# Optimization experiments

Hardware: AMD Instinct MI355X
Metric: run time of the kernel (lower is better)

The kernel has to match this reference:

```python
import jax, jax.numpy as jnp
import numpy as np

L = 4            # n_layers
D_MODEL = 768
D_STATE = 16
D_CONV = 4
EXPAND = 2
D_INNER = EXPAND * D_MODEL      # 1536
DT_RANK = (D_MODEL + 15) // 16  # 48
B = 2
T = 2048
LN_EPS = 1e-5


def setup_inputs() -> dict:
    key = jax.random.key(0)
    ks = jax.random.split(key, 12)
    s = 0.02
    x = jax.random.normal(ks[0], (B, T, D_MODEL), dtype=jnp.float32)
    in_proj_w = jax.random.normal(ks[1], (L, 2 * D_INNER, D_MODEL), dtype=jnp.float32) * s
    conv_w = jax.random.normal(ks[2], (L, D_INNER, D_CONV), dtype=jnp.float32) * s
    conv_b = jnp.zeros((L, D_INNER), dtype=jnp.float32)
    x_proj_w = jax.random.normal(ks[3], (L, DT_RANK + 2 * D_STATE, D_INNER), dtype=jnp.float32) * s
    dt_proj_w = jax.random.normal(ks[4], (L, D_INNER, DT_RANK), dtype=jnp.float32) * s
    dt_proj_b = jax.random.normal(ks[5], (L, D_INNER), dtype=jnp.float32) * 0.1
    # Standard S4D-real init: A = -[1..d_state], stored as log
    A_log = jnp.log(jnp.broadcast_to(
        jnp.arange(1, D_STATE + 1, dtype=jnp.float32), (L, D_INNER, D_STATE)))
    D_param = jnp.ones((L, D_INNER), dtype=jnp.float32)
    out_proj_w = jax.random.normal(ks[6], (L, D_MODEL, D_INNER), dtype=jnp.float32) * s
    ln_g = jnp.ones((L, D_MODEL), dtype=jnp.float32)
    ln_b = jnp.zeros((L, D_MODEL), dtype=jnp.float32)
    return {"x": x, "in_proj_w": in_proj_w, "conv_w": conv_w, "conv_b": conv_b,
            "x_proj_w": x_proj_w, "dt_proj_w": dt_proj_w, "dt_proj_b": dt_proj_b,
            "A_log": A_log, "D_param": D_param, "out_proj_w": out_proj_w,
            "ln_g": ln_g, "ln_b": ln_b}


def _layernorm(x, g, b):
    mu = jnp.mean(x, axis=-1, keepdims=True)
    var = jnp.mean(jnp.square(x - mu), axis=-1, keepdims=True)
    return (x - mu) * jax.lax.rsqrt(var + LN_EPS) * g + b


def _mamba_layer(x, inw, convw, convb, xpw, dtw, dtb, A_log, Dp, outw):
    # x: [B,T,d_model]
    Tn = x.shape[1]
    xz = jnp.einsum('btd,ed->bte', x, inw)          # [B,T,2*d_inner]
    xin, z = jnp.split(xz, 2, axis=-1)              # each [B,T,d_inner]
    # causal depthwise conv1d over time (kernel d_conv)
    xp = jnp.pad(xin, ((0, 0), (D_CONV - 1, 0), (0, 0)))
    xc = convb
    for k in range(D_CONV):
        xc = xc + xp[:, k:k + Tn, :] * convw[:, k]
    xc = jax.nn.silu(xc)                            # [B,T,d_inner]
    dbl = jnp.einsum('bti,ei->bte', xc, xpw)        # [B,T,dt_rank+2*d_state]
    dt, Bs, Cs = jnp.split(dbl, [DT_RANK, DT_RANK + D_STATE], axis=-1)
    dt = jax.nn.softplus(jnp.einsum('btr,dr->btd', dt, dtw) + dtb)  # [B,T,d_inner]
    A = -jnp.exp(A_log)                             # [d_inner,d_state]
    dA = jnp.exp(jnp.einsum('btd,dn->btdn', dt, A))  # discretized A
    dBu = (dt * xc)[..., None] * Bs[:, :, None, :]   # [B,T,d_inner,d_state]

    def step(h, inp):
        dA_t, dBu_t, C_t = inp                      # [B,d,n],[B,d,n],[B,n]
        h = dA_t * h + dBu_t
        y = jnp.einsum('bdn,bn->bd', h, C_t)
        return h, y

    h0 = jnp.zeros((x.shape[0], D_INNER, D_STATE), x.dtype)
    _, ys = jax.lax.scan(step, h0,
                         (jnp.swapaxes(dA, 0, 1), jnp.swapaxes(dBu, 0, 1),
                          jnp.swapaxes(Cs, 0, 1)))
    y = jnp.swapaxes(ys, 0, 1) + xc * Dp            # skip connection D*u
    y = y * jax.nn.silu(z)                          # gate
    return jnp.einsum('bti,ei->bte', y, outw)       # [B,T,d_model]


def reference(x, in_proj_w, conv_w, conv_b, x_proj_w, dt_proj_w, dt_proj_b,
              A_log, D_param, out_proj_w, ln_g, ln_b):
    for l in range(L):
        residual = x
        h = _mamba_layer(x, in_proj_w[l], conv_w[l], conv_b[l], x_proj_w[l],
                         dt_proj_w[l], dt_proj_b[l], A_log[l], D_param[l],
                         out_proj_w[l])
        h = _layernorm(h, ln_g[l], ln_b[l])
        x = h + residual                            # dropout=0 -> identity
    return x
```

## Files before the change

kernel.cpp:

```cpp
#include <hip/hip_runtime.h>

#define T_LEN 2048
#define DM    768
#define DI    1536
#define DS    16
#define BB    2
#define NROWS (BB * T_LEN)
#define NCH   128
#define CLEN  16

#define OFF_DTB 0
#define OFF_A   6144
#define OFF_DP  104448
#define OFF_CW  110592
#define OFF_CB  135168
#define OFF_LG  141312
#define OFF_LB  144384
#define PRM_TOT 147456

typedef __attribute__((ext_vector_type(8))) short bh8;
typedef __attribute__((ext_vector_type(4))) float f32x4;

typedef const __attribute__((address_space(1))) void as1_void;
typedef __attribute__((address_space(3))) void as3_void;

__device__ __forceinline__ void glds16(const void* g, void* l) {
    __builtin_amdgcn_global_load_lds((as1_void*)g, (as3_void*)l, 16, 0, 0);
}

__device__ __forceinline__ float bf2f(unsigned short u) {
    return __uint_as_float(((unsigned)u) << 16);
}
__device__ __forceinline__ unsigned short f2bf(float f) {
    unsigned u = __float_as_uint(f);
    u += 0x7FFFu + ((u >> 16) & 1u);
    return (unsigned short)(u >> 16);
}
__device__ __forceinline__ float ldin(const void* p, long i, int bf) {
    return bf ? bf2f(((const unsigned short*)p)[i]) : ((const float*)p)[i];
}

__global__ void k_sniff(const unsigned short* __restrict__ x, int* __restrict__ flag) {
    __shared__ int cnt[4];
    int tid = threadIdx.x;
    int local = 0;
#pragma unroll
    for (int j = 0; j < 4; ++j) {
        unsigned short u = x[tid * 4 + j];
        int e = (u >> 7) & 0xFF;
        if (e >= 100 && e <= 140) local++;
    }
    for (int off = 32; off; off >>= 1) local += __shfl_down(local, off, 64);
    if ((tid & 63) == 0) cnt[tid >> 6] = local;
    __syncthreads();
    if (tid == 0) {
        int tot = cnt[0] + cnt[1] + cnt[2] + cnt[3];
        *flag = (tot >= 900) ? 1 : 0;
    }
}

__global__ void k_conv_bf16(unsigned short* __restrict__ dst, const void* __restrict__ src,
                            long n, const int* __restrict__ flag) {
    int bf = *flag;
    long i = (long)blockIdx.x * 256 + threadIdx.x;
    if (i < n) dst[i] = bf ? ((const unsigned short*)src)[i] : f2bf(((const float*)src)[i]);
}

__global__ void k_convx(unsigned short* __restrict__ xbf, float* __restrict__ xf,
                        const void* __restrict__ src, const int* __restrict__ flag) {
    int bf = *flag;
    long i = (long)blockIdx.x * 256 + threadIdx.x;
    if (i < (long)NROWS * DM) {
        float v = ldin(src, i, bf);
        xbf[i] = f2bf(v);
        xf[i]  = v;
    }
}

__global__ void k_conv_xpw(unsigned short* __restrict__ dst, const void* __restrict__ src,
                           const int* __restrict__ flag) {
    int bf = *flag;
    long i = (long)blockIdx.x * 256 + threadIdx.x;
    const long total = 4L * 128 * 1536;
    if (i < total) {
        int c = (int)(i % 1536);
        long rl = i / 1536;
        int r = (int)(rl % 128);
        int l = (int)(rl / 128);
        unsigned short v = 0;
        if (r < 80) {
            long si = ((long)l * 80 + r) * 1536 + c;
            v = bf ? ((const unsigned short*)src)[si] : f2bf(((const float*)src)[si]);
        }
        dst[i] = v;
    }
}

__global__ void k_conv_dtw(unsigned short* __restrict__ dst, const void* __restrict__ src,
                           const int* __restrict__ flag) {
    int bf = *flag;
    long i = (long)blockIdx.x * 256 + threadIdx.x;
    const long total = 4L * 1536 * 64;
    if (i < total) {
        int c = (int)(i % 64);
        long rl = i / 64;
        int d = (int)(rl % 1536);
        int l = (int)(rl / 1536);
        unsigned short v = 0;
        if (c < 48) {
            long si = ((long)l * 1536 + d) * 48 + c;
            v = bf ? ((const unsigned short*)src)[si] : f2bf(((const float*)src)[si]);
        }
        dst[i] = v;
    }
}

__global__ void k_params(float* __restrict__ prm, const void* dtb, const void* alog,
                         const void* dpar, const void* cw, const void* cb,
                         const void* lg, const void* lb, const int* __restrict__ flag) {
    int bf = *flag;
    int i = blockIdx.x * 256 + threadIdx.x;
    if (i >= PRM_TOT) return;
    float v;
    if (i < OFF_A)        v = ldin(dtb, i - OFF_DTB, bf);
    else if (i < OFF_DP)  v = -__expf(ldin(alog, i - OFF_A, bf));
    else if (i < OFF_CW)  v = ldin(dpar, i - OFF_DP, bf);
    else if (i < OFF_CB)  v = ldin(cw, i - OFF_CW, bf);
    else if (i < OFF_LG)  v = ldin(cb, i - OFF_CB, bf);
    else if (i < OFF_LB)  v = ldin(lg, i - OFF_LG, bf);
    else                  v = ldin(lb, i - OFF_LB, bf);
    prm[i] = v;
}

__global__ __launch_bounds__(256) void k_gemm128(const unsigned short* __restrict__ A,
                                                 const unsigned short* __restrict__ B,
                                                 float* __restrict__ C,
                                                 int M, int N, int K) {
    __shared__ __align__(16) unsigned short As[128 * 32];
    __shared__ __align__(16) unsigned short Bs[128 * 32];
    const int tid = threadIdx.x;
    const int lane = tid & 63, wid = tid >> 6;
    const int wm = wid >> 1, wn = wid & 1;
    const long arow0 = (long)blockIdx.y * 128;
    const long bcol0 = (long)blockIdx.x * 128;
    const int r16 = lane >> 2;
    const int c8  = (lane & 3) * 8;
    f32x4 acc[4][4] = {};

    for (int k0 = 0; k0 < K; k0 += 32) {
#pragma unroll
        for (int j = 0; j < 2; ++j) {
            int chunk = wid + j * 4;
            int row = chunk * 16 + r16;
            glds16(&A[(arow0 + row) * K + k0 + c8], &As[chunk * 512]);
            glds16(&B[(bcol0 + row) * K + k0 + c8], &Bs[chunk * 512]);
        }
        __syncthreads();
        const int row = lane & 15, q8 = (lane >> 4) * 8;
        bh8 af[4], bfr[4];
#pragma unroll
        for (int i = 0; i < 4; ++i) af[i] = *(const bh8*)&As[(wm * 64 + i * 16 + row) * 32 + q8];
#pragma unroll
        for (int i = 0; i < 4; ++i) bfr[i] = *(const bh8*)&Bs[(wn * 64 + i * 16 + row) * 32 + q8];
#pragma unroll
        for (int i = 0; i < 4; ++i)
#pragma unroll
            for (int j = 0; j < 4; ++j)
                acc[i][j] = __builtin_amdgcn_mfma_f32_16x16x32_bf16(af[i], bfr[j], acc[i][j], 0, 0, 0);
        __syncthreads();
    }
    const int crow = (lane >> 4) * 4, ccol = lane & 15;
#pragma unroll
    for (int i = 0; i < 4; ++i)
#pragma unroll
        for (int j = 0; j < 4; ++j)
#pragma unroll
            for (int r = 0; r < 4; ++r) {
                long gr = arow0 + wm * 64 + i * 16 + crow + r;
                long gc = bcol0 + wn * 64 + j * 16 + ccol;
                C[gr * N + gc] = acc[i][j][r];
            }
}

template <int EPI>
__global__ __launch_bounds__(256) void k_gemm64(const unsigned short* __restrict__ A,
                                                const unsigned short* __restrict__ B,
                                                float* __restrict__ C,
                                                int M, int N, int K,
                                                const float* __restrict__ bias,
                                                unsigned short* __restrict__ dtlr) {
    __shared__ __align__(16) unsigned short As[64 * 32];
    __shared__ __align__(16) unsigned short Bs[64 * 32];
    const int tid = threadIdx.x;
    const int lane = tid & 63, wid = tid >> 6;
    const int wm = wid >> 1, wn = wid & 1;
    const long arow0 = (long)blockIdx.y * 64;
    const long bcol0 = (long)blockIdx.x * 64;
    const int r16 = lane >> 2;
    const int c8  = (lane & 3) * 8;
    f32x4 acc[2][2] = {};

    for (int k0 = 0; k0 < K; k0 += 32) {
        int row = wid * 16 + r16;
        glds16(&A[(arow0 + row) * K + k0 + c8], &As[wid * 512]);
        glds16(&B[(bcol0 + row) * K + k0 + c8], &Bs[wid * 512]);
        __syncthreads();
        const int row2 = lane & 15, q8 = (lane >> 4) * 8;
        bh8 af[2], bfr[2];
#pragma unroll
        for (int i = 0; i < 2; ++i) af[i] = *(const bh8*)&As[(wm * 32 + i * 16 + row2) * 32 + q8];
#pragma unroll
        for (int i = 0; i < 2; ++i) bfr[i] = *(const bh8*)&Bs[(wn * 32 + i * 16 + row2) * 32 + q8];
#pragma unroll
        for (int i = 0; i < 2; ++i)
#pragma unroll
            for (int j = 0; j < 2; ++j)
                acc[i][j] = __builtin_amdgcn_mfma_f32_16x16x32_bf16(af[i], bfr[j], acc[i][j], 0, 0, 0);
        __syncthreads();
    }
    const int crow = (lane >> 4) * 4, ccol = lane & 15;
#pragma unroll
    for (int i = 0; i < 2; ++i)
#pragma unroll
        for (int j = 0; j < 2; ++j)
#pragma unroll
            for (int r = 0; r < 4; ++r) {
                long gr = arow0 + wm * 32 + i * 16 + crow + r;
                long gc = bcol0 + wn * 32 + j * 16 + ccol;
                float v = acc[i][j][r];
                if (EPI == 1) {
                    v += bias[gc];
                    v = (v > 20.f) ? v : log1pf(__expf(v));
                }
                C[gr * N + gc] = v;
                if (EPI == 2) {
                    if (gc < 64) dtlr[gr * 64 + gc] = (gc < 48) ? f2bf(v) : (unsigned short)0;
                }
            }
}

__global__ __launch_bounds__(256) void k_conv(const float* __restrict__ xz,
                                              const float* __restrict__ cw,
                                              const float* __restrict__ cb,
                                              unsigned short* __restrict__ xcbf) {
    long i = (long)blockIdx.x * 256 + threadIdx.x;
    if (i >= (long)NROWS * DI) return;
    int d = (int)(i % DI);
    long bt = i / DI;
    int t = (int)(bt & (T_LEN - 1));
    float acc = cb[d];
#pragma unroll
    for (int k = 0; k < 4; ++k) {
        int ts = t + k - 3;
        if (ts >= 0) acc += xz[(bt + k - 3) * (2 * DI) + d] * cw[d * 4 + k];
    }
    float s = acc / (1.f + __expf(-acc));
    xcbf[i] = f2bf(s);
}

__global__ __launch_bounds__(256) void k_scan1(const float* __restrict__ dt,
                                               const unsigned short* __restrict__ xcbf,
                                               const float* __restrict__ dbl,
                                               const float* __restrict__ An,
                                               float* __restrict__ hch,
                                               float* __restrict__ sdtb) {
    const int tid = threadIdx.x;
    const int db = blockIdx.x % 6;
    const int c  = (blockIdx.x / 6) % NCH;
    const int b  = blockIdx.x / (6 * NCH);
    const int d  = db * 256 + tid;
    const int t0 = c * CLEN;
    float h[DS], An_r[DS];
    const f32x4* Ap = (const f32x4*)(An + (long)d * DS);
#pragma unroll
    for (int q = 0; q < 4; ++q) {
        f32x4 a4 = Ap[q];
#pragma unroll
        for (int j = 0; j < 4; ++j) { An_r[q * 4 + j] = a4[j]; h[q * 4 + j] = 0.f; }
    }
    float sdt = 0.f;
    const long rowb = (long)b * T_LEN + t0;
#pragma unroll 4
    for (int s = 0; s < CLEN; ++s) {
        long bt = rowb + s;
        float dtv = dt[bt * DI + d];
        float xcv = bf2f(xcbf[bt * DI + d]);
        int bi = __builtin_amdgcn_readfirstlane((int)(bt * 128 + 48));
        const f32x4* bp = (const f32x4*)(dbl + bi);
        float Bv[DS];
#pragma unroll
        for (int q = 0; q < 4; ++q) {
            f32x4 b4 = bp[q];
#pragma unroll
            for (int j = 0; j < 4; ++j) Bv[q * 4 + j] = b4[j];
        }
        float du = dtv * xcv;
        sdt += dtv;
#pragma unroll
        for (int n = 0; n < DS; ++n)
            h[n] = __expf(An_r[n] * dtv) * h[n] + du * Bv[n];
    }
    long o = (((long)b * NCH + c) * DI + d) * DS;
    f32x4* hp = (f32x4*)(hch + o);
#pragma unroll
    for (int q = 0; q < 4; ++q) {
        f32x4 h4;
#pragma unroll
        for (int j = 0; j < 4; ++j) h4[j] = h[q * 4 + j];
        hp[q] = h4;
    }
    sdtb[((long)b * NCH + c) * DI + d] = sdt;
}

__global__ __launch_bounds__(256) void k_scan2(float* __restrict__ hbuf,
                                               const float* __restrict__ sdtb,
                                               const float* __restrict__ An) {
    long gid = (long)blockIdx.x * 256 + threadIdx.x;
    if (gid >= (long)BB * DI * DS) return;
    int n = (int)(gid & 15);
    long r = gid >> 4;
    int d = (int)(r % DI);
    int b = (int)(r / DI);
    float an = An[(long)d * DS + n];
    float h = 0.f;
    for (int c = 0; c < NCH; ++c) {
        long idx = (((long)b * NCH + c) * DI + d) * DS + n;
        float p = __expf(an * sdtb[((long)b * NCH + c) * DI + d]);
        float g = hbuf[idx];
        hbuf[idx] = h;
        h = p * h + g;
    }
}

__global__ __launch_bounds__(256) void k_scan3(const float* __restrict__ dt,
                                               const unsigned short* __restrict__ xcbf,
                                               const float* __restrict__ dbl,
                                               const float* __restrict__ An,
                                               const float* __restrict__ Dp,
                                               const float* __restrict__ hin,
                                               const float* __restrict__ xz,
                                               unsigned short* __restrict__ ybf) {
    const int tid = threadIdx.x;
    const int db = blockIdx.x % 6;
    const int c  = (blockIdx.x / 6) % NCH;
    const int b  = blockIdx.x / (6 * NCH);
    const int d  = db * 256 + tid;
    const int t0 = c * CLEN;
    float h[DS], An_r[DS];
    long o = (((long)b * NCH + c) * DI + d) * DS;
    const f32x4* Ap = (const f32x4*)(An + (long)d * DS);
    const f32x4* Hp = (const f32x4*)(hin + o);
#pragma unroll
    for (int q = 0; q < 4; ++q) {
        f32x4 a4 = Ap[q], h4 = Hp[q];
#pragma unroll
        for (int j = 0; j < 4; ++j) { An_r[q * 4 + j] = a4[j]; h[q * 4 + j] = h4[j]; }
    }
    const float dcoef = Dp[d];
    const long rowb = (long)b * T_LEN + t0;
#pragma unroll 4
    for (int s = 0; s < CLEN; ++s) {
        long bt = rowb + s;
        float dtv = dt[bt * DI + d];
        float xcv = bf2f(xcbf[bt * DI + d]);
        int bi = __builtin_amdgcn_readfirstlane((int)(bt * 128 + 48));
        const f32x4* bp = (const f32x4*)(dbl + bi);
        float Bv[DS], Cv[DS];
#pragma unroll
        for (int q = 0; q < 4; ++q) {
            f32x4 b4 = bp[q], c4 = bp[q + 4];
#pragma unroll
            for (int j = 0; j < 4; ++j) { Bv[q * 4 + j] = b4[j]; Cv[q * 4 + j] = c4[j]; }
        }
        float du = dtv * xcv;
        float yp[4] = {xcv * dcoef, 0.f, 0.f, 0.f};
#pragma unroll
        for (int n = 0; n < DS; ++n) {
            h[n] = __expf(An_r[n] * dtv) * h[n] + du * Bv[n];
            yp[n & 3] += h[n] * Cv[n];
        }
        float y = (yp[0] + yp[1]) + (yp[2] + yp[3]);
        float zv = xz[bt * (2 * DI) + DI + d];
        y *= zv / (1.f + __expf(-zv));
        ybf[bt * DI + d] = f2bf(y);
    }
}

__global__ __launch_bounds__(256) void k_ln(const float* __restrict__ prj,
                                            float* __restrict__ x,
                                            unsigned short* __restrict__ xbf,
                                            const float* __restrict__ lg,
                                            const float* __restrict__ lb,
                                            void* __restrict__ dout,
                                            int is_last, const int* __restrict__ flag) {
    __shared__ float red[8];
    const int row = blockIdx.x;
    const int tid = threadIdx.x;
    float v[3];
    float s = 0.f, s2 = 0.f;
#pragma unroll
    for (int j = 0; j < 3; ++j) {
        v[j] = prj[(long)row * DM + tid + j * 256];
        s += v[j];
        s2 += v[j] * v[j];
    }
    for (int off = 32; off; off >>= 1) {
        s  += __shfl_down(s, off, 64);
        s2 += __shfl_down(s2, off, 64);
    }
    if ((tid & 63) == 0) { red[tid >> 6] = s; red[4 + (tid >> 6)] = s2; }
    __syncthreads();
    float S  = red[0] + red[1] + red[2] + red[3];
    float S2 = red[4] + red[5] + red[6] + red[7];
    float mu = S * (1.f / DM);
    float var = S2 * (1.f / DM) - mu * mu;
    float rs = rsqrtf(var + 1e-5f);
    int bf = *flag;
#pragma unroll
    for (int j = 0; j < 3; ++j) {
        int e = tid + j * 256;
        long idx = (long)row * DM + e;
        float out = (v[j] - mu) * rs * lg[e] + lb[e] + x[idx];
        x[idx] = out;
        xbf[idx] = f2bf(out);
        if (is_last) {
            if (bf) ((unsigned short*)dout)[idx] = f2bf(out);
            else    ((float*)dout)[idx] = out;
        }
    }
}

extern "C" void kernel_launch(void* const* d_in, const int* in_sizes, int n_in,
                              void* d_out, int out_size, void* d_ws, size_t ws_size,
                              hipStream_t stream) {
    char* ws = (char*)d_ws;
    const size_t O_FLAG = 0;
    const size_t O_WIN  = 256;
    const size_t O_WXP  = O_WIN + 18874368;
    const size_t O_WDT  = O_WXP + 1572864;
    const size_t O_WOUT = O_WDT + 786432;
    const size_t O_PRM  = O_WOUT + 9437184;
    const size_t O_XBF  = O_PRM + 589824;
    const size_t O_XF   = O_XBF + 6291456;
    const size_t O_XZ   = O_XF + 12582912;
    const size_t O_XCBF = O_XZ + 50331648;
    const size_t O_DBL  = O_XCBF + 12582912;
    const size_t O_DTLR = O_DBL + 2097152;
    const size_t O_DT   = O_DTLR + 524288;
    const size_t O_HCH  = O_DT + 25165824;
    const size_t O_SDT  = O_HCH + 25165824;
    const size_t O_YBF  = O_SDT + 1572864;

    int* flag = (int*)(ws + O_FLAG);
    unsigned short* Win  = (unsigned short*)(ws + O_WIN);
    unsigned short* Wxp  = (unsigned short*)(ws + O_WXP);
    unsigned short* Wdt  = (unsigned short*)(ws + O_WDT);
    unsigned short* Wout = (unsigned short*)(ws + O_WOUT);
    float* prm = (float*)(ws + O_PRM);
    unsigned short* Xbf = (unsigned short*)(ws + O_XBF);
    float* Xf  = (float*)(ws + O_XF);
    float* Xz  = (float*)(ws + O_XZ);
    unsigned short* Xcbf = (unsigned short*)(ws + O_XCBF);
    float* Dbl = (float*)(ws + O_DBL);
    unsigned short* Dtlr = (unsigned short*)(ws + O_DTLR);
    float* Dt  = (float*)(ws + O_DT);
    float* Hch = (float*)(ws + O_HCH);
    float* Sdt = (float*)(ws + O_SDT);
    unsigned short* Ybf = (unsigned short*)(ws + O_YBF);
    float* Prj = Xz;

    const void* in_x   = d_in[0];
    const void* in_inw = d_in[1];
    const void* in_xpw = d_in[4];
    const void* in_dtw = d_in[5];
    const void* in_ow  = d_in[9];

    k_sniff<<<1, 256, 0, stream>>>((const unsigned short*)in_x, flag);
    k_convx<<<12288, 256, 0, stream>>>(Xbf, Xf, in_x, flag);
    k_conv_bf16<<<36864, 256, 0, stream>>>(Win, in_inw, 9437184L, flag);
    k_conv_bf16<<<18432, 256, 0, stream>>>(Wout, in_ow, 4718592L, flag);
    k_conv_xpw<<<3072, 256, 0, stream>>>(Wxp, in_xpw, flag);
    k_conv_dtw<<<1536, 256, 0, stream>>>(Wdt, in_dtw, flag);
    k_params<<<576, 256, 0, stream>>>(prm, d_in[6], d_in[7], d_in[8], d_in[2], d_in[3],
                                      d_in[10], d_in[11], flag);

    for (int l = 0; l < 4; ++l) {
        const unsigned short* winL  = Win  + (size_t)l * 3072 * 768;
        const unsigned short* wxpL  = Wxp  + (size_t)l * 128 * 1536;
        const unsigned short* wdtL  = Wdt  + (size_t)l * 1536 * 64;
        const unsigned short* woutL = Wout + (size_t)l * 768 * 1536;
        const float* cwL  = prm + OFF_CW  + (size_t)l * DI * 4;
        const float* cbL  = prm + OFF_CB  + (size_t)l * DI;
        const float* dtbL = prm + OFF_DTB + (size_t)l * DI;
        const float* anL  = prm + OFF_A   + (size_t)l * DI * DS;
        const float* dpL  = prm + OFF_DP  + (size_t)l * DI;
        const float* lgL  = prm + OFF_LG  + (size_t)l * DM;
        const float* lbL  = prm + OFF_LB  + (size_t)l * DM;

        k_gemm128<<<dim3(24, 32), 256, 0, stream>>>(Xbf, winL, Xz, NROWS, 2 * DI, DM);
        k_conv<<<24576, 256, 0, stream>>>(Xz, cwL, cbL, Xcbf);
        k_gemm64<2><<<dim3(2, 64), 256, 0, stream>>>(Xcbf, wxpL, Dbl, NROWS, 128, DI, nullptr, Dtlr);
        k_gemm64<1><<<dim3(24, 64), 256, 0, stream>>>(Dtlr, wdtL, Dt, NROWS, DI, 64, dtbL, nullptr);
        k_scan1<<<BB * NCH * 6, 256, 0, stream>>>(Dt, Xcbf, Dbl, anL, Hch, Sdt);
        k_scan2<<<192, 256, 0, stream>>>(Hch, Sdt, anL);
        k_scan3<<<BB * NCH * 6, 256, 0, stream>>>(Dt, Xcbf, Dbl, anL, dpL, Hch, Xz, Ybf);
        k_gemm64<0><<<dim3(12, 64), 256, 0, stream>>>(Ybf, woutL, Prj, NROWS, DM, DI, nullptr, nullptr);
        k_ln<<<4096, 256, 0, stream>>>(Prj, Xf, Xbf, lgL, lbL, d_out, (l == 3) ? 1 : 0, flag);
    }
}
```

Baseline: 1.021 ms.

## Store intermediates in bf16, split-K x_proj, two-level chunk scan, tiled conv, fused prep

The in_proj output and dt are now stored in bf16 instead of fp32, which halves the intermediate traffic through conv and the scans. x_proj becomes a split-K GEMM that accumulates with atomicAdd into a zeroed buffer, giving more blocks for a skinny output. dt_proj now reads fp32 Dbl directly and converts it to bf16 in LDS, which removes the separate Dtlr buffer. The sequential inter-chunk scan is split into a segmented pass plus a short cross-segment pass to raise parallelism. The depthwise conv is tiled through LDS, and the six weight-prep kernels are merged into one launch. The costs are extra bf16 rounding of xz and dt, nondeterministic atomic summation, and an added memset.

```diff
diff --git a/kernel.cpp b/kernel.cpp
--- a/kernel.cpp
+++ b/kernel.cpp
@@ -8,6 +8,8 @@
 #define NROWS (BB * T_LEN)
 #define NCH   128
 #define CLEN  16
+#define NSEG  8
+#define SEGC  16
 
 #define OFF_DTB 0
 #define OFF_A   6144
@@ -59,30 +61,34 @@
     }
 }
 
-__global__ void k_conv_bf16(unsigned short* __restrict__ dst, const void* __restrict__ src,
-                            long n, const int* __restrict__ flag) {
+__global__ void k_prep(const void* in_x, const void* in_inw, const void* in_ow,
+                       const void* in_xpw, const void* in_dtw,
+                       const void* dtb, const void* alog, const void* dpar,
+                       const void* cw, const void* cb, const void* lg, const void* lb,
+                       unsigned short* __restrict__ xbf, float* __restrict__ xf,
+                       unsigned short* __restrict__ Win, unsigned short* __restrict__ Wout,
+                       unsigned short* __restrict__ Wxp, unsigned short* __restrict__ Wdt,
+                       float* __restrict__ prm, const int* __restrict__ flag) {
+    const long E0 = 3145728L;
+    const long E1 = E0 + 9437184L;
+    const long E2 = E1 + 4718592L;
+    const long E3 = E2 + 786432L;
+    const long E4 = E3 + 393216L;
+    const long E5 = E4 + 147456L;
     int bf = *flag;
-    long i = (long)blockIdx.x * 256 + threadIdx.x;
-    if (i < n) dst[i] = bf ? ((const unsigned short*)src)[i] : f2bf(((const float*)src)[i]);
-}
-
-__global__ void k_convx(unsigned short* __restrict__ xbf, float* __restrict__ xf,
-                        const void* __restrict__ src, const int* __restrict__ flag) {
-    int bf = *flag;
-    long i = (long)blockIdx.x * 256 + threadIdx.x;
-    if (i < (long)NROWS * DM) {
-        float v = ldin(src, i, bf);
-        xbf[i] = f2bf(v);
-        xf[i]  = v;
-    }
-}
-
-__global__ void k_conv_xpw(unsigned short* __restrict__ dst, const void* __restrict__ src,
-                           const int* __restrict__ flag) {
-    int bf = *flag;
-    long i = (long)blockIdx.x * 256 + threadIdx.x;
-    const long total = 4L * 128 * 1536;
-    if (i < total) {
+    long gid = (long)blockIdx.x * 256 + threadIdx.x;
+    if (gid < E0) {
+        float v = ldin(in_x, gid, bf);
+        xbf[gid] = f2bf(v);
+        xf[gid]  = v;
+    } else if (gid < E1) {
+        long i = gid - E0;
+        Win[i] = bf ? ((const unsigned short*)in_inw)[i] : f2bf(((const float*)in_inw)[i]);
+    } else if (gid < E2) {
+        long i = gid - E1;
+        Wout[i] = bf ? ((const unsigned short*)in_ow)[i] : f2bf(((const float*)in_ow)[i]);
+    } else if (gid < E3) {
+        long i = gid - E2;
         int c = (int)(i % 1536);
         long rl = i / 1536;
         int r = (int)(rl % 128);
@@ -90,18 +96,11 @@
         unsigned short v = 0;
         if (r < 80) {
             long si = ((long)l * 80 + r) * 1536 + c;
-            v = bf ? ((const unsigned short*)src)[si] : f2bf(((const float*)src)[si]);
-        }
-        dst[i] = v;
-    }
-}
-
-__global__ void k_conv_dtw(unsigned short* __restrict__ dst, const void* __restrict__ src,
-                           const int* __restrict__ flag) {
-    int bf = *flag;
-    long i = (long)blockIdx.x * 256 + threadIdx.x;
-    const long total = 4L * 1536 * 64;
-    if (i < total) {
+            v = bf ? ((const unsigned short*)in_xpw)[si] : f2bf(((const float*)in_xpw)[si]);
+        }
+        Wxp[i] = v;
+    } else if (gid < E4) {
+        long i = gid - E3;
         int c = (int)(i % 64);
         long rl = i / 64;
         int d = (int)(rl % 1536);
@@ -109,32 +108,26 @@
         unsigned short v = 0;
         if (c < 48) {
             long si = ((long)l * 1536 + d) * 48 + c;
-            v = bf ? ((const unsigned short*)src)[si] : f2bf(((const float*)src)[si]);
-        }
-        dst[i] = v;
-    }
-}
-
-__global__ void k_params(float* __restrict__ prm, const void* dtb, const void* alog,
-                         const void* dpar, const void* cw, const void* cb,
-                         const void* lg, const void* lb, const int* __restrict__ flag) {
-    int bf = *flag;
-    int i = blockIdx.x * 256 + threadIdx.x;
-    if (i >= PRM_TOT) return;
-    float v;
-    if (i < OFF_A)        v = ldin(dtb, i - OFF_DTB, bf);
-    else if (i < OFF_DP)  v = -__expf(ldin(alog, i - OFF_A, bf));
-    else if (i < OFF_CW)  v = ldin(dpar, i - OFF_DP, bf);
-    else if (i < OFF_CB)  v = ldin(cw, i - OFF_CW, bf);
-    else if (i < OFF_LG)  v = ldin(cb, i - OFF_CB, bf);
-    else if (i < OFF_LB)  v = ldin(lg, i - OFF_LG, bf);
-    else                  v = ldin(lb, i - OFF_LB, bf);
-    prm[i] = v;
+            v = bf ? ((const unsigned short*)in_dtw)[si] : f2bf(((const float*)in_dtw)[si]);
+        }
+        Wdt[i] = v;
+    } else if (gid < E5) {
+        int i = (int)(gid - E4);
+        float v;
+        if (i < OFF_A)        v = ldin(dtb, i - OFF_DTB, bf);
+        else if (i < OFF_DP)  v = -__expf(ldin(alog, i - OFF_A, bf));
+        else if (i < OFF_CW)  v = ldin(dpar, i - OFF_DP, bf);
+        else if (i < OFF_CB)  v = ldin(cw, i - OFF_CW, bf);
+        else if (i < OFF_LG)  v = ldin(cb, i - OFF_CB, bf);
+        else if (i < OFF_LB)  v = ldin(lg, i - OFF_LG, bf);
+        else                  v = ldin(lb, i - OFF_LB, bf);
+        prm[i] = v;
+    }
 }
 
 __global__ __launch_bounds__(256) void k_gemm128(const unsigned short* __restrict__ A,
                                                  const unsigned short* __restrict__ B,
-                                                 float* __restrict__ C,
+                                                 unsigned short* __restrict__ C,
                                                  int M, int N, int K) {
     __shared__ __align__(16) unsigned short As[128 * 32];
     __shared__ __align__(16) unsigned short Bs[128 * 32];
@@ -178,17 +171,134 @@
             for (int r = 0; r < 4; ++r) {
                 long gr = arow0 + wm * 64 + i * 16 + crow + r;
                 long gc = bcol0 + wn * 64 + j * 16 + ccol;
-                C[gr * N + gc] = acc[i][j][r];
+                C[gr * N + gc] = f2bf(acc[i][j][r]);
             }
 }
 
-template <int EPI>
-__global__ __launch_bounds__(256) void k_gemm64(const unsigned short* __restrict__ A,
-                                                const unsigned short* __restrict__ B,
-                                                float* __restrict__ C,
-                                                int M, int N, int K,
+__global__ __launch_bounds__(256) void k_xproj(const unsigned short* __restrict__ A,
+                                               const unsigned short* __restrict__ B,
+                                               float* __restrict__ C) {
+    __shared__ __align__(16) unsigned short As[64 * 32];
+    __shared__ __align__(16) unsigned short Bs[64 * 32];
+    const int tid = threadIdx.x;
+    const int lane = tid & 63, wid = tid >> 6;
+    const int wm = wid >> 1, wn = wid & 1;
+    const long arow0 = (long)blockIdx.y * 64;
+    const long bcol0 = (long)blockIdx.x * 64;
+    const int kbase = blockIdx.z * 384;
+    const int r16 = lane >> 2;
+    const int c8  = (lane & 3) * 8;
+    f32x4 acc[2][2] = {};
+
+    for (int kk = 0; kk < 384; kk += 32) {
+        int k0 = kbase + kk;
+        int row = wid * 16 + r16;
+        glds16(&A[(arow0 + row) * DI + k0 + c8], &As[wid * 512]);
+        glds16(&B[(bcol0 + row) * DI + k0 + c8], &Bs[wid * 512]);
+        __syncthreads();
+        const int row2 = lane & 15, q8 = (lane >> 4) * 8;
+        bh8 af[2], bfr[2];
+#pragma unroll
+        for (int i = 0; i < 2; ++i) af[i] = *(const bh8*)&As[(wm * 32 + i * 16 + row2) * 32 + q8];
+#pragma unroll
+        for (int i = 0; i < 2; ++i) bfr[i] = *(const bh8*)&Bs[(wn * 32 + i * 16 + row2) * 32 + q8];
+#pragma unroll
+        for (int i = 0; i < 2; ++i)
+#pragma unroll
+            for (int j = 0; j < 2; ++j)
+                acc[i][j] = __builtin_amdgcn_mfma_f32_16x16x32_bf16(af[i], bfr[j], acc[i][j], 0, 0, 0);
+        __syncthreads();
+    }
+    const int crow = (lane >> 4) * 4, ccol = lane & 15;
+#pragma unroll
+    for (int i = 0; i < 2; ++i)
+#pragma unroll
+        for (int j = 0; j < 2; ++j)
+#pragma unroll
+            for (int r = 0; r < 4; ++r) {
+                long gr = arow0 + wm * 32 + i * 16 + crow + r;
+                long gc = bcol0 + wn * 32 + j * 16 + ccol;
+                atomicAdd(&C[gr * 128 + gc], acc[i][j][r]);
+            }
+}
+
+__global__ __launch_bounds__(256) void k_dtproj(const float* __restrict__ Dbl,
+                                                const unsigned short* __restrict__ Wdt,
                                                 const float* __restrict__ bias,
-                                                unsigned short* __restrict__ dtlr) {
+                                                unsigned short* __restrict__ Dt) {
+    __shared__ __align__(16) unsigned short As[2 * 64 * 32];
+    __shared__ __align__(16) unsigned short Bs[2 * 64 * 32];
+    const int tid = threadIdx.x;
+    const int lane = tid & 63, wid = tid >> 6;
+    const int wm = wid >> 1, wn = wid & 1;
+    const long arow0 = (long)blockIdx.y * 64;
+    const long bcol0 = (long)blockIdx.x * 64;
+
+    {
+        int r = tid >> 2;
+        int cs = (tid & 3) * 16;
+        unsigned short tmp[16];
+#pragma unroll
+        for (int q = 0; q < 4; ++q) {
+            int col0 = cs + q * 4;
+            if (col0 < 48) {
+                f32x4 v = *(const f32x4*)&Dbl[(arow0 + r) * 128 + col0];
+#pragma unroll
+                for (int j = 0; j < 4; ++j) tmp[q * 4 + j] = f2bf(v[j]);
+            } else {
+#pragma unroll
+                for (int j = 0; j < 4; ++j) tmp[q * 4 + j] = 0;
+            }
+        }
+        int p = cs >> 5;
+        int cp = cs & 31;
+        *(bh8*)&As[p * 2048 + r * 32 + cp]     = *(bh8*)&tmp[0];
+        *(bh8*)&As[p * 2048 + r * 32 + cp + 8] = *(bh8*)&tmp[8];
+    }
+#pragma unroll
+    for (int j = 0; j < 2; ++j) {
+        int chunk = tid + j * 256;
+        int p = chunk >> 8;
+        int rem = chunk & 255;
+        int row = rem >> 2;
+        int c4 = rem & 3;
+        glds16(&Wdt[(bcol0 + row) * 64 + p * 32 + c4 * 8], &Bs[chunk * 8]);
+    }
+    __syncthreads();
+
+    const int row2 = lane & 15, q8 = (lane >> 4) * 8;
+    f32x4 acc[2][2] = {};
+#pragma unroll
+    for (int p = 0; p < 2; ++p) {
+        bh8 af[2], bfr[2];
+#pragma unroll
+        for (int i = 0; i < 2; ++i) af[i] = *(const bh8*)&As[p * 2048 + (wm * 32 + i * 16 + row2) * 32 + q8];
+#pragma unroll
+        for (int i = 0; i < 2; ++i) bfr[i] = *(const bh8*)&Bs[p * 2048 + (wn * 32 + i * 16 + row2) * 32 + q8];
+#pragma unroll
+        for (int i = 0; i < 2; ++i)
+#pragma unroll
+            for (int j = 0; j < 2; ++j)
+                acc[i][j] = __builtin_amdgcn_mfma_f32_16x16x32_bf16(af[i], bfr[j], acc[i][j], 0, 0, 0);
+    }
+    const int crow = (lane >> 4) * 4, ccol = lane & 15;
+#pragma unroll
+    for (int i = 0; i < 2; ++i)
+#pragma unroll
+        for (int j = 0; j < 2; ++j)
+#pragma unroll
+            for (int r = 0; r < 4; ++r) {
+                long gr = arow0 + wm * 32 + i * 16 + crow + r;
+                long gc = bcol0 + wn * 32 + j * 16 + ccol;
+                float v = acc[i][j][r] + bias[gc];
+                v = (v > 20.f) ? v : log1pf(__expf(v));
+                Dt[gr * DI + gc] = f2bf(v);
+            }
+}
+
+__global__ __launch_bounds__(256) void k_outproj(const unsigned short* __restrict__ A,
+                                                 const unsigned short* __restrict__ B,
+                                                 float* __restrict__ C) {
     __shared__ __align__(16) unsigned short As[64 * 32];
     __shared__ __align__(16) unsigned short Bs[64 * 32];
     const int tid = threadIdx.x;
@@ -200,10 +310,10 @@
     const int c8  = (lane & 3) * 8;
     f32x4 acc[2][2] = {};
 
-    for (int k0 = 0; k0 < K; k0 += 32) {
+    for (int k0 = 0; k0 < DI; k0 += 32) {
         int row = wid * 16 + r16;
-        glds16(&A[(arow0 + row) * K + k0 + c8], &As[wid * 512]);
-        glds16(&B[(bcol0 + row) * K + k0 + c8], &Bs[wid * 512]);
+        glds16(&A[(arow0 + row) * DI + k0 + c8], &As[wid * 512]);
+        glds16(&B[(bcol0 + row) * DI + k0 + c8], &Bs[wid * 512]);
         __syncthreads();
         const int row2 = lane & 15, q8 = (lane >> 4) * 8;
         bh8 af[2], bfr[2];
@@ -227,38 +337,40 @@
             for (int r = 0; r < 4; ++r) {
                 long gr = arow0 + wm * 32 + i * 16 + crow + r;
                 long gc = bcol0 + wn * 32 + j * 16 + ccol;
-                float v = acc[i][j][r];
-                if (EPI == 1) {
-                    v += bias[gc];
-                    v = (v > 20.f) ? v : log1pf(__expf(v));
-                }
-                C[gr * N + gc] = v;
-                if (EPI == 2) {
-                    if (gc < 64) dtlr[gr * 64 + gc] = (gc < 48) ? f2bf(v) : (unsigned short)0;
-                }
+                C[gr * DM + gc] = acc[i][j][r];
             }
 }
 
-__global__ __launch_bounds__(256) void k_conv(const float* __restrict__ xz,
+__global__ __launch_bounds__(256) void k_conv(const unsigned short* __restrict__ xz,
                                               const float* __restrict__ cw,
                                               const float* __restrict__ cb,
                                               unsigned short* __restrict__ xcbf) {
-    long i = (long)blockIdx.x * 256 + threadIdx.x;
-    if (i >= (long)NROWS * DI) return;
-    int d = (int)(i % DI);
-    long bt = i / DI;
-    int t = (int)(bt & (T_LEN - 1));
-    float acc = cb[d];
-#pragma unroll
-    for (int k = 0; k < 4; ++k) {
-        int ts = t + k - 3;
-        if (ts >= 0) acc += xz[(bt + k - 3) * (2 * DI) + d] * cw[d * 4 + k];
-    }
-    float s = acc / (1.f + __expf(-acc));
-    xcbf[i] = f2bf(s);
-}
-
-__global__ __launch_bounds__(256) void k_scan1(const float* __restrict__ dt,
+    __shared__ float tile[131 * 64];
+    const int tid = threadIdx.x;
+    const int d0 = blockIdx.x * 64;
+    const long t0 = (long)blockIdx.y * 128;
+    const bool seqstart = ((int)t0 & (T_LEN - 1)) == 0;
+    for (int j = tid; j < 131 * 64; j += 256) {
+        int row = j >> 6, col = j & 63;
+        float v = 0.f;
+        if (!(seqstart && row < 3)) v = bf2f(xz[(t0 - 3 + row) * (2 * DI) + d0 + col]);
+        tile[j] = v;
+    }
+    __syncthreads();
+    const int d = tid & 63, tl0 = tid >> 6;
+    const int dg = d0 + d;
+    const float w0 = cw[dg * 4 + 0], w1 = cw[dg * 4 + 1];
+    const float w2 = cw[dg * 4 + 2], w3 = cw[dg * 4 + 3];
+    const float bias = cb[dg];
+    for (int tt = tl0; tt < 128; tt += 4) {
+        float acc = bias + w0 * tile[tt * 64 + d] + w1 * tile[(tt + 1) * 64 + d]
+                         + w2 * tile[(tt + 2) * 64 + d] + w3 * tile[(tt + 3) * 64 + d];
+        float s = acc / (1.f + __expf(-acc));
+        xcbf[(t0 + tt) * DI + dg] = f2bf(s);
+    }
+}
+
+__global__ __launch_bounds__(256) void k_scan1(const unsigned short* __restrict__ dt,
                                                const unsigned short* __restrict__ xcbf,
                                                const float* __restrict__ dbl,
                                                const float* __restrict__ An,
@@ -283,7 +395,7 @@
 #pragma unroll 4
     for (int s = 0; s < CLEN; ++s) {
         long bt = rowb + s;
-        float dtv = dt[bt * DI + d];
+        float dtv = bf2f(dt[bt * DI + d]);
         float xcv = bf2f(xcbf[bt * DI + d]);
         int bi = __builtin_amdgcn_readfirstlane((int)(bt * 128 + 48));
         const f32x4* bp = (const f32x4*)(dbl + bi);
@@ -312,33 +424,65 @@
     sdtb[((long)b * NCH + c) * DI + d] = sdt;
 }
 
-__global__ __launch_bounds__(256) void k_scan2(float* __restrict__ hbuf,
-                                               const float* __restrict__ sdtb,
-                                               const float* __restrict__ An) {
+__global__ __launch_bounds__(256) void k_scan2a(float* __restrict__ hbuf,
+                                                const float* __restrict__ sdtb,
+                                                const float* __restrict__ An,
+                                                float* __restrict__ cum,
+                                                float* __restrict__ Gseg,
+                                                float* __restrict__ Sseg) {
     long gid = (long)blockIdx.x * 256 + threadIdx.x;
-    if (gid >= (long)BB * DI * DS) return;
     int n = (int)(gid & 15);
-    long r = gid >> 4;
-    int d = (int)(r % DI);
-    int b = (int)(r / DI);
+    long t = gid >> 4;
+    int d  = (int)(t % DI);
+    int sg = (int)((t / DI) & (NSEG - 1));
+    int b  = (int)(t / (DI * NSEG));
     float an = An[(long)d * DS + n];
-    float h = 0.f;
-    for (int c = 0; c < NCH; ++c) {
-        long idx = (((long)b * NCH + c) * DI + d) * DS + n;
-        float p = __expf(an * sdtb[((long)b * NCH + c) * DI + d]);
+    float h = 0.f, cs = 0.f;
+    for (int i = 0; i < SEGC; ++i) {
+        int c = sg * SEGC + i;
+        long rowi = ((long)b * NCH + c) * DI + d;
+        long idx = rowi * DS + n;
+        float sdt = sdtb[rowi];
         float g = hbuf[idx];
         hbuf[idx] = h;
-        h = p * h + g;
-    }
-}
-
-__global__ __launch_bounds__(256) void k_scan3(const float* __restrict__ dt,
+        if (n == 0) cum[rowi] = cs;
+        h = __expf(an * sdt) * h + g;
+        cs += sdt;
+    }
+    long gi = (((long)b * NSEG + sg) * DI + d) * DS + n;
+    Gseg[gi] = h;
+    if (n == 0) Sseg[((long)b * NSEG + sg) * DI + d] = cs;
+}
+
+__global__ __launch_bounds__(256) void k_scan2b(const float* __restrict__ Gseg,
+                                                const float* __restrict__ Sseg,
+                                                const float* __restrict__ An,
+                                                float* __restrict__ Hseg) {
+    long gid = (long)blockIdx.x * 256 + threadIdx.x;
+    int n = (int)(gid & 15);
+    long t = gid >> 4;
+    int d = (int)(t % DI);
+    int b = (int)(t / DI);
+    float an = An[(long)d * DS + n];
+    float H = 0.f;
+    for (int sg = 0; sg < NSEG; ++sg) {
+        long gi = (((long)b * NSEG + sg) * DI + d) * DS + n;
+        float G = Gseg[gi];
+        float S = Sseg[((long)b * NSEG + sg) * DI + d];
+        Hseg[gi] = H;
+        H = __expf(an * S) * H + G;
+    }
+}
+
+__global__ __launch_bounds__(256) void k_scan3(const unsigned short* __restrict__ dt,
                                                const unsigned short* __restrict__ xcbf,
                                                const float* __restrict__ dbl,
                                                const float* __restrict__ An,
                                                const float* __restrict__ Dp,
-                                               const float* __restrict__ hin,
-                                               const float* __restrict__ xz,
+                                               const float* __restrict__ hpref,
+                                               const float* __restrict__ cum,
+                                               const float* __restrict__ Hseg,
+                                               const unsigned short* __restrict__ xz,
                                                unsigned short* __restrict__ ybf) {
     const int tid = threadIdx.x;
     const int db = blockIdx.x % 6;
@@ -346,22 +490,31 @@
     const int b  = blockIdx.x / (6 * NCH);
     const int d  = db * 256 + tid;
     const int t0 = c * CLEN;
+    const int sg = c / SEGC;
     float h[DS], An_r[DS];
-    long o = (((long)b * NCH + c) * DI + d) * DS;
+    long rowi = ((long)b * NCH + c) * DI + d;
+    long o = rowi * DS;
+    long gi = (((long)b * NSEG + sg) * DI + d) * DS;
+    const float cs = cum[rowi];
     const f32x4* Ap = (const f32x4*)(An + (long)d * DS);
-    const f32x4* Hp = (const f32x4*)(hin + o);
+    const f32x4* Pp = (const f32x4*)(hpref + o);
+    const f32x4* Hp = (const f32x4*)(Hseg + gi);
 #pragma unroll
     for (int q = 0; q < 4; ++q) {
-        f32x4 a4 = Ap[q], h4 = Hp[q];
-#pragma unroll
-        for (int j = 0; j < 4; ++j) { An_r[q * 4 + j] = a4[j]; h[q * 4 + j] = h4[j]; }
+        f32x4 a4 = Ap[q], p4 = Pp[q], h4 = Hp[q];
+#pragma unroll
+        for (int j = 0; j < 4; ++j) {
+            int n = q * 4 + j;
+            An_r[n] = a4[j];
+            h[n] = __expf(a4[j] * cs) * h4[j] + p4[j];
+        }
     }
     const float dcoef = Dp[d];
     const long rowb = (long)b * T_LEN + t0;
 #pragma unroll 4
     for (int s = 0; s < CLEN; ++s) {
         long bt = rowb + s;
-        float dtv = dt[bt * DI + d];
+        float dtv = bf2f(dt[bt * DI + d]);
         float xcv = bf2f(xcbf[bt * DI + d]);
         int bi = __builtin_amdgcn_readfirstlane((int)(bt * 128 + 48));
         const f32x4* bp = (const f32x4*)(dbl + bi);
@@ -380,7 +533,7 @@
             yp[n & 3] += h[n] * Cv[n];
         }
         float y = (yp[0] + yp[1]) + (yp[2] + yp[3]);
-        float zv = xz[bt * (2 * DI) + DI + d];
+        float zv = bf2f(xz[bt * (2 * DI) + DI + d]);
         y *= zv / (1.f + __expf(-zv));
         ybf[bt * DI + d] = f2bf(y);
     }
@@ -436,20 +589,23 @@
     char* ws = (char*)d_ws;
     const size_t O_FLAG = 0;
     const size_t O_WIN  = 256;
-    const size_t O_WXP  = O_WIN + 18874368;
-    const size_t O_WDT  = O_WXP + 1572864;
-    const size_t O_WOUT = O_WDT + 786432;
+    const size_t O_WXP  = O_WIN  + 18874368;
+    const size_t O_WDT  = O_WXP  + 1572864;
+    const size_t O_WOUT = O_WDT  + 786432;
     const size_t O_PRM  = O_WOUT + 9437184;
-    const size_t O_XBF  = O_PRM + 589824;
-    const size_t O_XF   = O_XBF + 6291456;
-    const size_t O_XZ   = O_XF + 12582912;
-    const size_t O_XCBF = O_XZ + 50331648;
+    const size_t O_XBF  = O_PRM  + 589824;
+    const size_t O_XF   = O_XBF  + 6291456;
+    const size_t O_XZ   = O_XF   + 12582912;
+    const size_t O_XCBF = O_XZ   + 25165824;
     const size_t O_DBL  = O_XCBF + 12582912;
-    const size_t O_DTLR = O_DBL + 2097152;
-    const size_t O_DT   = O_DTLR + 524288;
-    const size_t O_HCH  = O_DT + 25165824;
-    const size_t O_SDT  = O_HCH + 25165824;
-    const size_t O_YBF  = O_SDT + 1572864;
+    const size_t O_DT   = O_DBL  + 2097152;
+    const size_t O_HCH  = O_DT   + 12582912;
+    const size_t O_SDT  = O_HCH  + 25165824;
+    const size_t O_CUM  = O_SDT  + 1572864;
+    const size_t O_GSEG = O_CUM  + 1572864;
+    const size_t O_SSEG = O_GSEG + 1572864;
+    const size_t O_HSEG = O_SSEG + 98304;
+    const size_t O_YBF  = O_HSEG + 1572864;
 
     int* flag = (int*)(ws + O_FLAG);
     unsigned short* Win  = (unsigned short*)(ws + O_WIN);
@@ -459,30 +615,24 @@
     float* prm = (float*)(ws + O_PRM);
     unsigned short* Xbf = (unsigned short*)(ws + O_XBF);
     float* Xf  = (float*)(ws + O_XF);
-    float* Xz  = (float*)(ws + O_XZ);
+    unsigned short* Xz = (unsigned short*)(ws + O_XZ);
     unsigned short* Xcbf = (unsigned short*)(ws + O_XCBF);
     float* Dbl = (float*)(ws + O_DBL);
-    unsigned short* Dtlr = (unsigned short*)(ws + O_DTLR);
-    float* Dt  = (float*)(ws + O_DT);
+    unsigned short* Dt = (unsigned short*)(ws + O_DT);
     float* Hch = (float*)(ws + O_HCH);
     float* Sdt = (float*)(ws + O_SDT);
+    float* Cum = (float*)(ws + O_CUM);
+    float* Gsg = (float*)(ws + O_GSEG);
+    float* Ssg = (float*)(ws + O_SSEG);
+    float* Hsg = (float*)(ws + O_HSEG);
     unsigned short* Ybf = (unsigned short*)(ws + O_YBF);
-    float* Prj = Xz;
-
-    const void* in_x   = d_in[0];
-    const void* in_inw = d_in[1];
-    const void* in_xpw = d_in[4];
-    const void* in_dtw = d_in[5];
-    const void* in_ow  = d_in[9];
-
-    k_sniff<<<1, 256, 0, stream>>>((const unsigned short*)in_x, flag);
-    k_convx<<<12288, 256, 0, stream>>>(Xbf, Xf, in_x, flag);
-    k_conv_bf16<<<36864, 256, 0, stream>>>(Win, in_inw, 9437184L, flag);
-    k_conv_bf16<<<18432, 256, 0, stream>>>(Wout, in_ow, 4718592L, flag);
-    k_conv_xpw<<<3072, 256, 0, stream>>>(Wxp, in_xpw, flag);
-    k_conv_dtw<<<1536, 256, 0, stream>>>(Wdt, in_dtw, flag);
-    k_params<<<576, 256, 0, stream>>>(prm, d_in[6], d_in[7], d_in[8], d_in[2], d_in[3],
-                                      d_in[10], d_in[11], flag);
+    float* Prj = (float*)(ws + O_XZ);
+
+    k_sniff<<<1, 256, 0, stream>>>((const unsigned short*)d_in[0], flag);
+    k_prep<<<72768, 256, 0, stream>>>(d_in[0], d_in[1], d_in[9], d_in[4], d_in[5],
+                                      d_in[6], d_in[7], d_in[8], d_in[2], d_in[3],
+                                      d_in[10], d_in[11],
+                                      Xbf, Xf, Win, Wout, Wxp, Wdt, prm, flag);
 
     for (int l = 0; l < 4; ++l) {
         const unsigned short* winL  = Win  + (size_t)l * 3072 * 768;
@@ -498,13 +648,15 @@
         const float* lbL  = prm + OFF_LB  + (size_t)l * DM;
 
         k_gemm128<<<dim3(24, 32), 256, 0, stream>>>(Xbf, winL, Xz, NROWS, 2 * DI, DM);
-        k_conv<<<24576, 256, 0, stream>>>(Xz, cwL, cbL, Xcbf);
-        k_gemm64<2><<<dim3(2, 64), 256, 0, stream>>>(Xcbf, wxpL, Dbl, NROWS, 128, DI, nullptr, Dtlr);
-        k_gemm64<1><<<dim3(24, 64), 256, 0, stream>>>(Dtlr, wdtL, Dt, NROWS, DI, 64, dtbL, nullptr);
+        k_conv<<<dim3(24, 32), 256, 0, stream>>>(Xz, cwL, cbL, Xcbf);
+        hipMemsetAsync(Dbl, 0, 2097152, stream);
+        k_xproj<<<dim3(2, 64, 4), 256, 0, stream>>>(Xcbf, wxpL, Dbl);
+        k_dtproj<<<dim3(24, 64), 256, 0, stream>>>(Dbl, wdtL, dtbL, Dt);
         k_scan1<<<BB * NCH * 6, 256, 0, stream>>>(Dt, Xcbf, Dbl, anL, Hch, Sdt);
-        k_scan2<<<192, 256, 0, stream>>>(Hch, Sdt, anL);
-        k_scan3<<<BB * NCH * 6, 256, 0, stream>>>(Dt, Xcbf, Dbl, anL, dpL, Hch, Xz, Ybf);
-        k_gemm64<0><<<dim3(12, 64), 256, 0, stream>>>(Ybf, woutL, Prj, NROWS, DM, DI, nullptr, nullptr);
+        k_scan2a<<<1536, 256, 0, stream>>>(Hch, Sdt, anL, Cum, Gsg, Ssg);
+        k_scan2b<<<192, 256, 0, stream>>>(Gsg, Ssg, anL, Hsg);
+        k_scan3<<<BB * NCH * 6, 256, 0, stream>>>(Dt, Xcbf, Dbl, anL, dpL, Hch, Cum, Hsg, Xz, Ybf);
+        k_outproj<<<dim3(12, 64), 256, 0, stream>>>(Ybf, woutL, Prj);
         k_ln<<<4096, 256, 0, stream>>>(Prj, Xf, Xbf, lgL, lbL, d_out, (l == 3) ? 1 : 0, flag);
     }
 }
```

Result: faster. 912.0 us (-10.7%).
